# Performance work log

Hardware: AMD Instinct MI355X
Metric: run time of the kernel (lower is better)

## Reference

```python
import jax, jax.numpy as jnp
import numpy as np
import math

B, C, H, W, S = 8, 512, 64, 64, 4


def setup_inputs() -> dict:
    key = jax.random.key(0)
    ks = jax.random.split(key, 7)
    s = 1.0 / math.sqrt(C)  # ~ torch Linear init scale
    x = jax.random.normal(ks[0], (B, C, H, W), jnp.float32)
    Wq = jax.random.uniform(ks[1], (C, C), jnp.float32, -s, s)
    bq = jax.random.uniform(ks[2], (C,), jnp.float32, -s, s)
    Wk = jax.random.uniform(ks[3], (C, C), jnp.float32, -s, s)
    bk = jax.random.uniform(ks[4], (C,), jnp.float32, -s, s)
    Wv = jax.random.uniform(ks[5], (C, C), jnp.float32, -s, s)
    bv = jax.random.uniform(ks[6], (C,), jnp.float32, -s, s)
    return {"x": x, "Wq": Wq, "bq": bq, "Wk": Wk, "bk": bk, "Wv": Wv, "bv": bv}


def reference(x, Wq, bq, Wk, bk, Wv, bv):
    # x: (B, C, H, W). Faithful to the torch module's output, but expressed
    # in the algebraically-equivalent efficient form: the repeat_interleaved
    # attention matrix A is block-constant, so out = repeat(A_m @ Vsum).
    b, c, h, w = x.shape
    nb = (h // S) * (w // S)  # number of SxS spatial blocks
    hw = h * w
    ss = S * S

    # Block means in unfold order (bh, bw): (B, nb, C)
    x_avg = x.reshape(b, c, h // S, S, w // S, S).mean(axis=(3, 5))
    x_avg = x_avg.reshape(b, c, nb).transpose(0, 2, 1)

    Q = x_avg @ Wq.T + bq  # (B, nb, C)
    K = x_avg @ Wk.T + bk  # (B, nb, C)
    A = jax.nn.softmax(jnp.einsum('bnc,bmc->bnm', Q, K) / jnp.sqrt(jnp.float32(c)), axis=-1)

    # V over flat row-major pixels: (B, HW, C)
    x_flat = x.reshape(b, c, hw).transpose(0, 2, 1)
    V = x_flat @ Wv.T + bv

    # repeat_interleave on dim=2 means column group j of A sums V rows
    # [j*ss, (j+1)*ss) in FLAT pixel order (not spatial blocks) - faithful.
    Vsum = V.reshape(b, hw // ss, ss, c).sum(axis=2)  # (B, nb, C)
    out_small = jnp.einsum('bnm,bmc->bnc', A, Vsum)   # (B, nb, C)
    # repeat_interleave on dim=1: each block row broadcast to ss flat pixels
    out_flat = jnp.repeat(out_small, ss, axis=1)      # (B, HW, C)
    return out_flat.transpose(0, 2, 1).reshape(b, c, h, w)
```

## Files before the change

### kernel.cpp

```cpp
#include <hip/hip_runtime.h>

typedef __attribute__((ext_vector_type(8))) short short8;
typedef __attribute__((ext_vector_type(4))) float f32x4;

__device__ __forceinline__ unsigned short f2bf(float f) {
    union { float f; unsigned int i; } v; v.f = f;
    unsigned int x = v.i;
    return (unsigned short)((x + 0x7FFFu + ((x >> 16) & 1u)) >> 16);
}
__device__ __forceinline__ f32x4 mfma16(short8 a, short8 b, f32x4 c) {
    return __builtin_amdgcn_mfma_f32_16x16x32_bf16(a, b, c, 0, 0, 0);
}

__global__ void prep_kernel(const float* __restrict__ x,
                            const float* __restrict__ Wq,
                            const float* __restrict__ Wk,
                            const float* __restrict__ Wv,
                            unsigned short* __restrict__ xavg,
                            unsigned short* __restrict__ xsum,
                            unsigned short* __restrict__ Wb)
{
    const int blk = blockIdx.x;
    const int t = threadIdx.x;
    if (blk >= 4096) {
        const int i = (blk - 4096) * 256 + t;
        const int m = i >> 15;
        const int o = (i & 32767) * 8;
        const float* src = (m == 0) ? Wq : (m == 1) ? Wk : Wv;
        unsigned short* dst = Wb + m * 262144 + o;
        float4 a = *(const float4*)(src + o);
        float4 b = *(const float4*)(src + o + 4);
        *(ushort4*)(dst)     = make_ushort4(f2bf(a.x), f2bf(a.y), f2bf(a.z), f2bf(a.w));
        *(ushort4*)(dst + 4) = make_ushort4(f2bf(b.x), f2bf(b.y), f2bf(b.z), f2bf(b.w));
        return;
    }
    const int b = blk >> 9;
    const int c = blk & 511;

    const float4* p = (const float4*)(x + (size_t)blk * 4096) + t * 4;
    float4 a0 = p[0], a1 = p[1], a2 = p[2], a3 = p[3];
    float s0 = a0.x + a0.y + a0.z + a0.w;
    float s1 = a1.x + a1.y + a1.z + a1.w;
    float s2 = a2.x + a2.y + a2.z + a2.w;
    float s3 = a3.x + a3.y + a3.z + a3.w;

    xsum[((size_t)b * 256 + t) * 512 + c] = f2bf(s0 + s1 + s2 + s3);

    __shared__ float part[1024];
    ((float4*)part)[t] = make_float4(s0, s1, s2, s3);
    __syncthreads();

    const int bh = t >> 4, bw = t & 15;
    float m = (part[(bh * 4 + 0) * 16 + bw] + part[(bh * 4 + 1) * 16 + bw] +
               part[(bh * 4 + 2) * 16 + bw] + part[(bh * 4 + 3) * 16 + bw]) * 0.0625f;
    xavg[((size_t)b * 256 + t) * 512 + c] = f2bf(m);
}

__global__ void proj_gemm(const unsigned short* __restrict__ xavg,
                          const unsigned short* __restrict__ xsum,
                          const unsigned short* __restrict__ Wb,
                          const float* __restrict__ bq,
                          const float* __restrict__ bk,
                          const float* __restrict__ bv,
                          unsigned short* __restrict__ QK,
                          unsigned short* __restrict__ VsT)
{
    const int blk = blockIdx.x;
    const int lane = threadIdx.x & 63, quad = lane >> 4, r16 = lane & 15;
    const int w = threadIdx.x >> 6;

    if (blk < 512) {
        const int wave = blk * 4 + w;
        const int mt2 = wave >> 5, nt2 = wave & 31;
        const unsigned short* xp0 = xavg + (size_t)(mt2 * 32 + r16) * 512 + quad * 8;
        const unsigned short* xp1 = xp0 + 16 * 512;
        const unsigned short* wp0 = Wb + (size_t)(nt2 * 32 + r16) * 512 + quad * 8;
        const unsigned short* wp1 = wp0 + 16 * 512;

        f32x4 acc00 = {0,0,0,0}, acc01 = acc00, acc10 = acc00, acc11 = acc00;
#pragma unroll 4
        for (int k = 0; k < 512; k += 32) {
            short8 a0 = *(const short8*)(xp0 + k);
            short8 a1 = *(const short8*)(xp1 + k);
            short8 b0 = *(const short8*)(wp0 + k);
            short8 b1 = *(const short8*)(wp1 + k);
            acc00 = mfma16(a0, b0, acc00);
            acc01 = mfma16(a0, b1, acc01);
            acc10 = mfma16(a1, b0, acc10);
            acc11 = mfma16(a1, b1, acc11);
        }
        const int c0 = nt2 * 32 + r16, c1 = c0 + 16;
        const float bias0 = (c0 < 512) ? bq[c0] : bk[c0 - 512];
        const float bias1 = (c1 < 512) ? bq[c1] : bk[c1 - 512];
        const int row0 = mt2 * 32 + quad * 4;
#pragma unroll
        for (int r = 0; r < 4; ++r) {
            QK[(size_t)(row0 + r) * 1024 + c0]      = f2bf(acc00[r] + bias0);
            QK[(size_t)(row0 + r) * 1024 + c1]      = f2bf(acc01[r] + bias1);
            QK[(size_t)(row0 + 16 + r) * 1024 + c0] = f2bf(acc10[r] + bias0);
            QK[(size_t)(row0 + 16 + r) * 1024 + c1] = f2bf(acc11[r] + bias1);
        }
    } else {
        const int vblk = blk - 512;
        const int b = vblk >> 5;
        const int wave = (vblk & 31) * 4 + w;
        const int mt2 = wave >> 4, nt2 = wave & 15;
        const unsigned short* xp0 = xsum + (size_t)b * 131072 + (size_t)(mt2 * 32 + r16) * 512 + quad * 8;
        const unsigned short* xp1 = xp0 + 16 * 512;
        const unsigned short* wp0 = Wb + 524288 + (size_t)(nt2 * 32 + r16) * 512 + quad * 8;
        const unsigned short* wp1 = wp0 + 16 * 512;

        f32x4 acc00 = {0,0,0,0}, acc01 = acc00, acc10 = acc00, acc11 = acc00;
#pragma unroll 4
        for (int k = 0; k < 512; k += 32) {
            short8 a0 = *(const short8*)(xp0 + k);
            short8 a1 = *(const short8*)(xp1 + k);
            short8 b0 = *(const short8*)(wp0 + k);
            short8 b1 = *(const short8*)(wp1 + k);
            acc00 = mfma16(a0, b0, acc00);
            acc01 = mfma16(a0, b1, acc01);
            acc10 = mfma16(a1, b0, acc10);
            acc11 = mfma16(a1, b1, acc11);
        }
        const int c0 = nt2 * 32 + r16, c1 = c0 + 16;
        const float bias0 = 16.f * bv[c0], bias1 = 16.f * bv[c1];
        unsigned short* vb = VsT + (size_t)b * 131072;
        const int m0 = mt2 * 32 + quad * 4;
#pragma unroll
        for (int r = 0; r < 4; ++r) {
            vb[(size_t)c0 * 256 + m0 + r]      = f2bf(acc00[r] + bias0);
            vb[(size_t)c1 * 256 + m0 + r]      = f2bf(acc01[r] + bias1);
            vb[(size_t)c0 * 256 + m0 + 16 + r] = f2bf(acc10[r] + bias0);
            vb[(size_t)c1 * 256 + m0 + 16 + r] = f2bf(acc11[r] + bias1);
        }
    }
}

__global__ void attn_out(const unsigned short* __restrict__ QK,
                         const unsigned short* __restrict__ VsT,
                         float* __restrict__ out)
{
    __shared__ float S[32][257];
    __shared__ unsigned short Abf[32 * 264];
    const int b = blockIdx.y;
    const int strip = blockIdx.x >> 2;
    const int cq = blockIdx.x & 3;
    const int w = threadIdx.x >> 6, lane = threadIdx.x & 63;
    const int quad = lane >> 4, r16 = lane & 15;

    const unsigned short* qp0 = QK + (size_t)(b * 256 + strip * 32 + r16) * 1024 + quad * 8;
    const unsigned short* qp1 = qp0 + 16 * 1024;
#pragma unroll
    for (int g = 0; g < 2; ++g) {
        const int ct = w * 2 + g;
        const unsigned short* kp0 = QK + (size_t)(b * 256 + ct * 32 + r16) * 1024 + 512 + quad * 8;
        const unsigned short* kp1 = kp0 + 16 * 1024;
        f32x4 acc00 = {0,0,0,0}, acc01 = acc00, acc10 = acc00, acc11 = acc00;
#pragma unroll 4
        for (int k = 0; k < 512; k += 32) {
            short8 a0 = *(const short8*)(qp0 + k);
            short8 a1 = *(const short8*)(qp1 + k);
            short8 b0 = *(const short8*)(kp0 + k);
            short8 b1 = *(const short8*)(kp1 + k);
            acc00 = mfma16(a0, b0, acc00);
            acc01 = mfma16(a0, b1, acc01);
            acc10 = mfma16(a1, b0, acc10);
            acc11 = mfma16(a1, b1, acc11);
        }
        const int col0 = ct * 32 + r16;
#pragma unroll
        for (int r = 0; r < 4; ++r) {
            S[quad * 4 + r][col0]           = acc00[r];
            S[quad * 4 + r][col0 + 16]      = acc01[r];
            S[quad * 4 + 16 + r][col0]      = acc10[r];
            S[quad * 4 + 16 + r][col0 + 16] = acc11[r];
        }
    }
    __syncthreads();

    {
        const int t = threadIdx.x;
        const int r = t >> 3, seg = t & 7;
        float v[32];
        float mx = -3.4e38f;
#pragma unroll
        for (int j = 0; j < 32; ++j) {
            v[j] = S[r][seg * 32 + j] * 0.044194173824159216f;
            mx = fmaxf(mx, v[j]);
        }
        mx = fmaxf(mx, __shfl_xor(mx, 1));
        mx = fmaxf(mx, __shfl_xor(mx, 2));
        mx = fmaxf(mx, __shfl_xor(mx, 4));
        float sum = 0.f;
#pragma unroll
        for (int j = 0; j < 32; ++j) { v[j] = __expf(v[j] - mx); sum += v[j]; }
        sum += __shfl_xor(sum, 1);
        sum += __shfl_xor(sum, 2);
        sum += __shfl_xor(sum, 4);
        const float inv = 1.f / sum;
        unsigned short* ap = Abf + r * 264 + seg * 32;
#pragma unroll
        for (int j = 0; j < 32; j += 4)
            *(ushort4*)(ap + j) = make_ushort4(f2bf(v[j] * inv), f2bf(v[j + 1] * inv),
                                               f2bf(v[j + 2] * inv), f2bf(v[j + 3] * inv));
    }
    __syncthreads();

    const int cbase = cq * 128 + w * 32;
    const unsigned short* ap0 = Abf + r16 * 264 + quad * 8;
    const unsigned short* ap1 = ap0 + 16 * 264;
    const unsigned short* vp0 = VsT + (size_t)b * 131072 + (size_t)(cbase + r16) * 256 + quad * 8;
    const unsigned short* vp1 = vp0 + 16 * 256;

    f32x4 acc00 = {0,0,0,0}, acc01 = acc00, acc10 = acc00, acc11 = acc00;
#pragma unroll 4
    for (int k = 0; k < 256; k += 32) {
        short8 a0 = *(const short8*)(ap0 + k);
        short8 a1 = *(const short8*)(ap1 + k);
        short8 b0 = *(const short8*)(vp0 + k);
        short8 b1 = *(const short8*)(vp1 + k);
        acc00 = mfma16(a0, b0, acc00);
        acc01 = mfma16(a0, b1, acc01);
        acc10 = mfma16(a1, b0, acc10);
        acc11 = mfma16(a1, b1, acc11);
    }
    const int c0 = cbase + r16, c1 = c0 + 16;
    float* ob0 = out + (size_t)(b * 512 + c0) * 4096;
    float* ob1 = out + (size_t)(b * 512 + c1) * 4096;
    const int n0 = strip * 32 + quad * 4;
#pragma unroll
    for (int r = 0; r < 4; ++r) {
        float4 q;
        float4* d;
        q = make_float4(acc00[r], acc00[r], acc00[r], acc00[r]);
        d = (float4*)(ob0 + (n0 + r) * 16);      d[0] = q; d[1] = q; d[2] = q; d[3] = q;
        q = make_float4(acc01[r], acc01[r], acc01[r], acc01[r]);
        d = (float4*)(ob1 + (n0 + r) * 16);      d[0] = q; d[1] = q; d[2] = q; d[3] = q;
        q = make_float4(acc10[r], acc10[r], acc10[r], acc10[r]);
        d = (float4*)(ob0 + (n0 + 16 + r) * 16); d[0] = q; d[1] = q; d[2] = q; d[3] = q;
        q = make_float4(acc11[r], acc11[r], acc11[r], acc11[r]);
        d = (float4*)(ob1 + (n0 + 16 + r) * 16); d[0] = q; d[1] = q; d[2] = q; d[3] = q;
    }
}

extern "C" void kernel_launch(void* const* d_in, const int* in_sizes, int n_in,
                              void* d_out, int out_size, void* d_ws, size_t ws_size,
                              hipStream_t stream) {
    const float* x  = (const float*)d_in[0];
    const float* Wq = (const float*)d_in[1];
    const float* bq = (const float*)d_in[2];
    const float* Wk = (const float*)d_in[3];
    const float* bk = (const float*)d_in[4];
    const float* Wv = (const float*)d_in[5];
    const float* bv = (const float*)d_in[6];
    float* out = (float*)d_out;

    unsigned short* Wb   = (unsigned short*)d_ws;
    unsigned short* xavg = Wb + 786432;
    unsigned short* xsum = xavg + 1048576;
    unsigned short* QK   = xsum + 1048576;
    unsigned short* VsT  = QK + 2097152;

    prep_kernel<<<4480, 256, 0, stream>>>(x, Wq, Wk, Wv, xavg, xsum, Wb);
    proj_gemm<<<768, 256, 0, stream>>>(xavg, xsum, Wb, bq, bk, bv, QK, VsT);
    attn_out<<<dim3(32, 8), 256, 0, stream>>>(QK, VsT, out);
}
```

Baseline: 193.2 us.

## Double attn_out grid and stage output tile in shared memory for coalesced stores

```diff
diff --git a/kernel.cpp b/kernel.cpp
--- a/kernel.cpp
+++ b/kernel.cpp
@@ -142,9 +142,11 @@
 {
     __shared__ float S[32][257];
     __shared__ unsigned short Abf[32 * 264];
+    float (*osT)[33] = (float(*)[33])&S[0][0];
+
     const int b = blockIdx.y;
-    const int strip = blockIdx.x >> 2;
-    const int cq = blockIdx.x & 3;
+    const int strip = blockIdx.x >> 3;
+    const int cq = blockIdx.x & 7;
     const int w = threadIdx.x >> 6, lane = threadIdx.x & 63;
     const int quad = lane >> 4, r16 = lane & 15;
 
@@ -206,40 +208,41 @@
     }
     __syncthreads();
 
-    const int cbase = cq * 128 + w * 32;
-    const unsigned short* ap0 = Abf + r16 * 264 + quad * 8;
-    const unsigned short* ap1 = ap0 + 16 * 264;
-    const unsigned short* vp0 = VsT + (size_t)b * 131072 + (size_t)(cbase + r16) * 256 + quad * 8;
-    const unsigned short* vp1 = vp0 + 16 * 256;
-
-    f32x4 acc00 = {0,0,0,0}, acc01 = acc00, acc10 = acc00, acc11 = acc00;
-#pragma unroll 4
-    for (int k = 0; k < 256; k += 32) {
-        short8 a0 = *(const short8*)(ap0 + k);
-        short8 a1 = *(const short8*)(ap1 + k);
-        short8 b0 = *(const short8*)(vp0 + k);
-        short8 b1 = *(const short8*)(vp1 + k);
-        acc00 = mfma16(a0, b0, acc00);
-        acc01 = mfma16(a0, b1, acc01);
-        acc10 = mfma16(a1, b0, acc10);
-        acc11 = mfma16(a1, b1, acc11);
-    }
-    const int c0 = cbase + r16, c1 = c0 + 16;
-    float* ob0 = out + (size_t)(b * 512 + c0) * 4096;
-    float* ob1 = out + (size_t)(b * 512 + c1) * 4096;
-    const int n0 = strip * 32 + quad * 4;
-#pragma unroll
-    for (int r = 0; r < 4; ++r) {
-        float4 q;
-        float4* d;
-        q = make_float4(acc00[r], acc00[r], acc00[r], acc00[r]);
-        d = (float4*)(ob0 + (n0 + r) * 16);      d[0] = q; d[1] = q; d[2] = q; d[3] = q;
-        q = make_float4(acc01[r], acc01[r], acc01[r], acc01[r]);
-        d = (float4*)(ob1 + (n0 + r) * 16);      d[0] = q; d[1] = q; d[2] = q; d[3] = q;
-        q = make_float4(acc10[r], acc10[r], acc10[r], acc10[r]);
-        d = (float4*)(ob0 + (n0 + 16 + r) * 16); d[0] = q; d[1] = q; d[2] = q; d[3] = q;
-        q = make_float4(acc11[r], acc11[r], acc11[r], acc11[r]);
-        d = (float4*)(ob1 + (n0 + 16 + r) * 16); d[0] = q; d[1] = q; d[2] = q; d[3] = q;
+    {
+        const int ch = w * 16 + r16;
+        const unsigned short* ap0 = Abf + r16 * 264 + quad * 8;
+        const unsigned short* ap1 = ap0 + 16 * 264;
+        const unsigned short* vp  = VsT + (size_t)b * 131072 +
+                                    (size_t)(cq * 64 + ch) * 256 + quad * 8;
+        f32x4 acc0 = {0,0,0,0}, acc1 = acc0;
+#pragma unroll 4
+        for (int k = 0; k < 256; k += 32) {
+            short8 a0 = *(const short8*)(ap0 + k);
+            short8 a1 = *(const short8*)(ap1 + k);
+            short8 b0 = *(const short8*)(vp + k);
+            acc0 = mfma16(a0, b0, acc0);
+            acc1 = mfma16(a1, b0, acc1);
+        }
+#pragma unroll
+        for (int r = 0; r < 4; ++r) {
+            osT[ch][quad * 4 + r]      = acc0[r];
+            osT[ch][quad * 4 + 16 + r] = acc1[r];
+        }
+    }
+    __syncthreads();
+
+    {
+        const int t = threadIdx.x;
+        const int ch2 = t >> 7;
+        const int j = t & 127;
+        const int n = j >> 2;
+        float* obase = out + (size_t)(b * 512 + cq * 64) * 4096 + strip * 512 + j * 4;
+#pragma unroll
+        for (int it = 0; it < 32; ++it) {
+            const int ch = it * 2 + ch2;
+            const float v = osT[ch][n];
+            *(float4*)(obase + (size_t)ch * 4096) = make_float4(v, v, v, v);
+        }
     }
 }
 
@@ -263,5 +266,5 @@
 
     prep_kernel<<<4480, 256, 0, stream>>>(x, Wq, Wk, Wv, xavg, xsum, Wb);
     proj_gemm<<<768, 256, 0, stream>>>(xavg, xsum, Wb, bq, bk, bv, QK, VsT);
-    attn_out<<<dim3(32, 8), 256, 0, stream>>>(QK, VsT, out);
-}
+    attn_out<<<dim3(64, 8), 256, 0, stream>>>(QK, VsT, out);
+}
```

New measurement: 193.0 us. About the same (-0.1%).
